# Optimization experiments

Measured on AMD Instinct MI355X. Metric: run time of the kernel, lower is better.

## Reference

```python
import jax, jax.numpy as jnp
import numpy as np

PATCH = 16

def setup_inputs() -> dict:
    key = jax.random.key(0)
    k1, k2, k3, k4, k5 = jax.random.split(key, 5)
    B, C, H, W = 128, 3, 224, 224
    N = (H // PATCH) * (W // PATCH)  # 196
    D = 768
    x = jax.random.normal(k1, (B, C, H, W), dtype=jnp.float32)
    ys = jax.random.randint(k2, (B, N), 0, H - PATCH + 1, dtype=jnp.int64)
    xs = jax.random.randint(k3, (B, N), 0, W - PATCH + 1, dtype=jnp.int64)
    W_proj = jax.random.normal(k4, (D, C * PATCH * PATCH), dtype=jnp.float32) * 0.02
    b_proj = jax.random.normal(k5, (D,), dtype=jnp.float32) * 0.02
    return {"x": x, "ys": ys, "xs": xs, "W_proj": W_proj, "b_proj": b_proj}

def reference(x, ys, xs, W_proj, b_proj):
    # x: [B, C, H, W]; ys, xs: [B, N] top-left patch coords
    B, C, H, W = x.shape
    N = ys.shape[1]
    P = PATCH
    # flattened within-patch offsets: d[p] = dy*W + dx, shape [P*P]
    dy = jnp.arange(P)[:, None]
    dx = jnp.arange(P)[None, :]
    d = (dy * W + dx).reshape(-1)  # [P*P]
    base = ys * W + xs                         # [B, N]
    indices = base[:, :, None] + d[None, None, :]  # [B, N, P*P]
    indices = indices.reshape(B, N * P * P)
    # gather over flattened spatial dims for every channel
    x_flat = x.reshape(B, C, H * W)
    patches = jnp.take_along_axis(
        x_flat, indices[:, None, :].astype(jnp.int32), axis=2
    )  # [B, C, N*P*P]
    patches = patches.reshape(B, C, N, P * P)
    patches = patches.transpose(0, 2, 1, 3).reshape(B, N, C * P * P)  # [B, N, C*P*P]
    patch_tokens = jnp.einsum('bnf,df->bnd', patches, W_proj) + b_proj  # [B, N, D]
    patch_positions = jnp.stack([ys, xs], axis=-1)  # [B, N, 2]
    return (patch_tokens, patch_positions)
```

## Files before the change

kernel.cpp:

```cpp
#include <hip/hip_runtime.h>
#include <hip/hip_bf16.h>

#define B_IMG   128
#define CH      3
#define HW      224
#define NPATCH  196
#define TOKENS  25088
#define PATCH   16
#define FDIM    768
#define DDIM    768
#define TOKELEMS ((size_t)TOKENS * FDIM)
#define OUT_TOKENS ((size_t)TOKENS * DDIM)

#define GATHER_BRICK_BLOCKS (37632 / 4)
#define W_BRICK_BLOCKS      (1152 / 4)

typedef short short8 __attribute__((ext_vector_type(8)));
typedef float f32x4  __attribute__((ext_vector_type(4)));

static __device__ __forceinline__ unsigned short f2bf(float v) {
  unsigned u = __float_as_uint(v);
  unsigned r = u + 0x7fffu + ((u >> 16) & 1u);
  return (unsigned short)(r >> 16);
}

__global__ __launch_bounds__(256) void prep_kernel(
    const float* __restrict__ x, const int* __restrict__ ys,
    const int* __restrict__ xs, const float* __restrict__ W,
    short* __restrict__ PF, short* __restrict__ WF,
    float* __restrict__ pos) {
  const int w  = threadIdx.x >> 6;
  const int l  = threadIdx.x & 63;
  const int lr = l & 15;
  const int lg = l >> 4;
  const int k8rem = lg & 3;

  if (blockIdx.x < GATHER_BRICK_BLOCKS) {
    const int brick  = blockIdx.x * 4 + w;
    const int tile16 = brick / 24;
    const int kt     = brick - tile16 * 24;
    const int tok    = tile16 * 16 + lr;
    const int b      = tok / NPATCH;
    const int y      = ys[tok];
    const int xc     = xs[tok];
    const int k8     = kt * 4 + k8rem;
    const int c      = k8 >> 5;
    const int rem    = k8 & 31;
    const int py     = rem >> 1;
    const int px0    = (rem & 1) * 8;
    const float* src = x + (size_t)(b * CH + c) * (HW * HW) +
                       (size_t)(y + py) * HW + xc + px0;
    float4 v0 = *(const float4*)src;
    float4 v1 = *(const float4*)(src + 4);
    short8 o;
    o[0] = (short)f2bf(v0.x); o[1] = (short)f2bf(v0.y);
    o[2] = (short)f2bf(v0.z); o[3] = (short)f2bf(v0.w);
    o[4] = (short)f2bf(v1.x); o[5] = (short)f2bf(v1.y);
    o[6] = (short)f2bf(v1.z); o[7] = (short)f2bf(v1.w);
    *(short8*)&PF[(size_t)brick * 512 + l * 8] = o;
    if (kt == 0 && lg == 0) {
      pos[(size_t)tok * 2]     = (float)y;
      pos[(size_t)tok * 2 + 1] = (float)xc;
    }
  } else {
    const int brick  = (blockIdx.x - GATHER_BRICK_BLOCKS) * 4 + w;
    const int tile16 = brick / 24;
    const int kt     = brick - tile16 * 24;
    const int n      = tile16 * 16 + lr;
    const int k8     = kt * 4 + k8rem;
    const float* src = W + (size_t)n * FDIM + k8 * 8;
    float4 v0 = *(const float4*)src;
    float4 v1 = *(const float4*)(src + 4);
    short8 o;
    o[0] = (short)f2bf(v0.x); o[1] = (short)f2bf(v0.y);
    o[2] = (short)f2bf(v0.z); o[3] = (short)f2bf(v0.w);
    o[4] = (short)f2bf(v1.x); o[5] = (short)f2bf(v1.y);
    o[6] = (short)f2bf(v1.z); o[7] = (short)f2bf(v1.w);
    *(short8*)&WF[(size_t)brick * 512 + l * 8] = o;
  }
}

__global__ __launch_bounds__(256) void gemm_kernel(
    const short* __restrict__ PF,
    const short* __restrict__ WF,
    const float* __restrict__ bias,
    float* __restrict__ C) {
  const int tid = threadIdx.x;
  const int w   = tid >> 6;
  const int l   = tid & 63;
  const int lr  = l & 15;
  const int lg  = l >> 4;

  const int id  = blockIdx.x;
  const int nid = (id & 7) * 147 + (id >> 3);
  const int job = nid * 4 + w;
  const int mt  = job / 12;
  const int nt  = job - mt * 12;
  const int m0  = mt * 64;
  const int n0  = nt * 64;

  const short* pA = PF + (size_t)(m0 >> 4) * 24 * 512 + l * 8;
  const short* pB = WF + (size_t)(n0 >> 4) * 24 * 512 + l * 8;

  float bs4[4];
#pragma unroll
  for (int ni = 0; ni < 4; ++ni) bs4[ni] = bias[n0 + ni * 16 + lr];
#pragma unroll
  for (int ni = 0; ni < 4; ++ni) asm volatile("" : "+v"(bs4[ni]));

  f32x4 acc[4][4];
  const f32x4 z = {0.f, 0.f, 0.f, 0.f};
#pragma unroll
  for (int mi = 0; mi < 4; ++mi)
#pragma unroll
    for (int ni = 0; ni < 4; ++ni) acc[mi][ni] = z;

  short8 A0[4], B0[4], A1[4], B1[4];

#define LOADSET(Af, Bf, KT)                                                  \
  do {                                                                       \
    const size_t ko_ = (size_t)(KT) * 512;                                   \
    _Pragma("unroll")                                                        \
    for (int i = 0; i < 4; ++i)                                              \
      Af[i] = *(const short8*)(pA + (size_t)i * 12288 + ko_);                \
    _Pragma("unroll")                                                        \
    for (int i = 0; i < 4; ++i)                                              \
      Bf[i] = *(const short8*)(pB + (size_t)i * 12288 + ko_);                \
  } while (0)

#define MFMASET(Af, Bf)                                                      \
  do {                                                                       \
    __builtin_amdgcn_s_setprio(1);                                           \
    _Pragma("unroll")                                                        \
    for (int mi = 0; mi < 4; ++mi)                                           \
      _Pragma("unroll")                                                      \
      for (int ni = 0; ni < 4; ++ni)                                         \
        acc[mi][ni] = __builtin_amdgcn_mfma_f32_16x16x32_bf16(               \
            Af[mi], Bf[ni], acc[mi][ni], 0, 0, 0);                           \
    __builtin_amdgcn_s_setprio(0);                                           \
  } while (0)

  LOADSET(A0, B0, 0);
#pragma unroll 1
  for (int s = 0; s < 24; s += 2) {
    LOADSET(A1, B1, s + 1);
    asm volatile("s_waitcnt vmcnt(8)" ::: "memory");
    MFMASET(A0, B0);
    const int k2 = (s + 2 < 24) ? s + 2 : 0;
    LOADSET(A0, B0, k2);
    asm volatile("s_waitcnt vmcnt(8)" ::: "memory");
    MFMASET(A1, B1);
  }

#pragma unroll
  for (int ni = 0; ni < 4; ++ni) {
    const int col = n0 + ni * 16 + lr;
#pragma unroll
    for (int mi = 0; mi < 4; ++mi) {
      const int row = m0 + mi * 16 + lg * 4;
      const f32x4 v = acc[mi][ni];
#pragma unroll
      for (int j = 0; j < 4; ++j)
        C[(size_t)(row + j) * DDIM + col] = v[j] + bs4[ni];
    }
  }
#undef LOADSET
#undef MFMASET
}

__global__ __launch_bounds__(256) void naive_kernel(
    const float* __restrict__ x, const int* __restrict__ ys,
    const int* __restrict__ xs, const float* __restrict__ W,
    const float* __restrict__ bias, float* __restrict__ out) {
  __shared__ float prow[FDIM];
  const int tok = blockIdx.x;
  const int t   = threadIdx.x;
  const int b   = tok / NPATCH;
  const int y   = ys[tok];
  const int xc  = xs[tok];
  for (int i = t; i < FDIM; i += 256) {
    int c = i >> 8, rem = i & 255, py = rem >> 4, px = rem & 15;
    prow[i] = x[((size_t)(b * CH + c) * HW + y + py) * HW + xc + px];
  }
  __syncthreads();
  for (int dd = 0; dd < 3; ++dd) {
    const int d = t + dd * 256;
    float s = bias[d];
    const float4* wr = (const float4*)&W[(size_t)d * FDIM];
    const float4* pr = (const float4*)prow;
    for (int f4 = 0; f4 < FDIM / 4; ++f4) {
      float4 wv = wr[f4];
      float4 pv = pr[f4];
      s += wv.x * pv.x + wv.y * pv.y + wv.z * pv.z + wv.w * pv.w;
    }
    out[(size_t)tok * DDIM + d] = s;
  }
  if (t == 0) {
    float* pos = out + OUT_TOKENS;
    pos[(size_t)tok * 2]     = (float)y;
    pos[(size_t)tok * 2 + 1] = (float)xc;
  }
}

extern "C" void kernel_launch(void* const* d_in, const int* in_sizes, int n_in,
                              void* d_out, int out_size, void* d_ws, size_t ws_size,
                              hipStream_t stream) {
  const float* x    = (const float*)d_in[0];
  const int*   ys   = (const int*)d_in[1];
  const int*   xs   = (const int*)d_in[2];
  const float* W    = (const float*)d_in[3];
  const float* bias = (const float*)d_in[4];
  float* out = (float*)d_out;
  float* pos = out + OUT_TOKENS;

  const size_t w_bytes = (size_t)DDIM * FDIM * 2;
  const size_t p_bytes = TOKELEMS * 2;
  if (ws_size >= w_bytes + p_bytes) {
    short* WF = (short*)d_ws;
    short* PF = (short*)d_ws + (size_t)DDIM * FDIM;
    prep_kernel<<<GATHER_BRICK_BLOCKS + W_BRICK_BLOCKS, 256, 0, stream>>>(
        x, ys, xs, W, PF, WF, pos);
    gemm_kernel<<<1176, 256, 0, stream>>>(PF, WF, bias, out);
  } else {
    naive_kernel<<<TOKENS, 256, 0, stream>>>(x, ys, xs, W, bias, out);
  }
}
```

Baseline: 75.66 us.

## Share A tiles across waves via LDS triple buffer, enlarge block tile to 128x256

The GEMM moves from independent 64x64 per-wave tiles loaded straight from global memory to a 128x256 block tile. The A operand is staged through a three-slot LDS buffer with direct global-to-LDS loads and shared by all four waves, while each wave keeps its own B fragments in registers. The grid halves and the XCD-aware block mapping is adjusted to the new count. This cuts redundant global/L2 traffic for A, at the cost of more accumulator registers (32 f32x4), per-step barriers, and lower occupancy.

```diff
diff --git a/kernel.cpp b/kernel.cpp
--- a/kernel.cpp
+++ b/kernel.cpp
@@ -22,6 +22,13 @@
   unsigned u = __float_as_uint(v);
   unsigned r = u + 0x7fffu + ((u >> 16) & 1u);
   return (unsigned short)(r >> 16);
+}
+
+static __device__ __forceinline__ void gload16(const short* g, short* l) {
+  __builtin_amdgcn_global_load_lds(
+      (const __attribute__((address_space(1))) void*)g,
+      (__attribute__((address_space(3))) void*)l,
+      16, 0, 0);
 }
 
 __global__ __launch_bounds__(256) void prep_kernel(
@@ -85,22 +92,26 @@
     const short* __restrict__ WF,
     const float* __restrict__ bias,
     float* __restrict__ C) {
+  __shared__ short Ab[3][8 * 512];
+
   const int tid = threadIdx.x;
   const int w   = tid >> 6;
   const int l   = tid & 63;
   const int lr  = l & 15;
   const int lg  = l >> 4;
 
-  const int id  = blockIdx.x;
-  const int nid = (id & 7) * 147 + (id >> 3);
-  const int job = nid * 4 + w;
-  const int mt  = job / 12;
-  const int nt  = job - mt * 12;
-  const int m0  = mt * 64;
-  const int n0  = nt * 64;
-
-  const short* pA = PF + (size_t)(m0 >> 4) * 24 * 512 + l * 8;
+  const int id   = blockIdx.x;
+  const int xcd  = id & 7;
+  const int chnk = id >> 3;
+  const int nid  = (xcd < 4 ? xcd * 74 : 296 + (xcd - 4) * 73) + chnk;
+  const int mtB  = nid / 3;
+  const int ntg  = nid - mtB * 3;
+  const int m0   = mtB * 128;
+  const int n0   = ntg * 256 + w * 64;
+
   const short* pB = WF + (size_t)(n0 >> 4) * 24 * 512 + l * 8;
+  const short* pAs = PF + (size_t)(mtB * 8 + w * 2) * 24 * 512 + l * 8;
+  const int ldst = (w * 2) * 512;
 
   float bs4[4];
 #pragma unroll
@@ -108,55 +119,92 @@
 #pragma unroll
   for (int ni = 0; ni < 4; ++ni) asm volatile("" : "+v"(bs4[ni]));
 
-  f32x4 acc[4][4];
+  f32x4 acc[8][4];
   const f32x4 z = {0.f, 0.f, 0.f, 0.f};
 #pragma unroll
-  for (int mi = 0; mi < 4; ++mi)
+  for (int mi = 0; mi < 8; ++mi)
 #pragma unroll
     for (int ni = 0; ni < 4; ++ni) acc[mi][ni] = z;
 
-  short8 A0[4], B0[4], A1[4], B1[4];
-
-#define LOADSET(Af, Bf, KT)                                                  \
-  do {                                                                       \
-    const size_t ko_ = (size_t)(KT) * 512;                                   \
-    _Pragma("unroll")                                                        \
-    for (int i = 0; i < 4; ++i)                                              \
-      Af[i] = *(const short8*)(pA + (size_t)i * 12288 + ko_);                \
-    _Pragma("unroll")                                                        \
-    for (int i = 0; i < 4; ++i)                                              \
-      Bf[i] = *(const short8*)(pB + (size_t)i * 12288 + ko_);                \
+  short8 B0[4], B1[4];
+
+#define LOADB(BR, KT)                                                      \
+  do {                                                                     \
+    _Pragma("unroll")                                                      \
+    for (int i = 0; i < 4; ++i)                                            \
+      BR[i] = *(const short8*)(pB + (size_t)i * 12288 + (size_t)(KT) * 512);\
   } while (0)
 
-#define MFMASET(Af, Bf)                                                      \
-  do {                                                                       \
-    __builtin_amdgcn_s_setprio(1);                                           \
-    _Pragma("unroll")                                                        \
-    for (int mi = 0; mi < 4; ++mi)                                           \
-      _Pragma("unroll")                                                      \
-      for (int ni = 0; ni < 4; ++ni)                                         \
-        acc[mi][ni] = __builtin_amdgcn_mfma_f32_16x16x32_bf16(               \
-            Af[mi], Bf[ni], acc[mi][ni], 0, 0, 0);                           \
-    __builtin_amdgcn_s_setprio(0);                                           \
+#define STAGEA(SLOT, KT)                                                   \
+  do {                                                                     \
+    gload16(pAs + (size_t)(KT) * 512, &Ab[(SLOT)][ldst]);                  \
+    gload16(pAs + 12288 + (size_t)(KT) * 512, &Ab[(SLOT)][ldst + 512]);    \
   } while (0)
 
-  LOADSET(A0, B0, 0);
+#define GSTEP(BUF, STG, BR, KT2, DOSTG, DOB, VMN)                          \
+  do {                                                                     \
+    short8 a_[4];                                                          \
+    _Pragma("unroll")                                                      \
+    for (int i = 0; i < 4; ++i)                                            \
+      a_[i] = *(const short8*)&Ab[(BUF)][i * 512 + l * 8];                 \
+    if (DOSTG) STAGEA(STG, KT2);                                           \
+    asm volatile("s_waitcnt vmcnt(" #VMN ")" ::: "memory");                \
+    __builtin_amdgcn_sched_barrier(0);                                     \
+    __builtin_amdgcn_s_setprio(1);                                         \
+    _Pragma("unroll")                                                      \
+    for (int mi = 0; mi < 4; ++mi)                                         \
+      _Pragma("unroll")                                                    \
+      for (int ni = 0; ni < 4; ++ni)                                       \
+        acc[mi][ni] = __builtin_amdgcn_mfma_f32_16x16x32_bf16(             \
+            a_[mi], BR[ni], acc[mi][ni], 0, 0, 0);                         \
+    __builtin_amdgcn_s_setprio(0);                                         \
+    short8 a2_[4];                                                         \
+    _Pragma("unroll")                                                      \
+    for (int i = 0; i < 4; ++i)                                            \
+      a2_[i] = *(const short8*)&Ab[(BUF)][(4 + i) * 512 + l * 8];          \
+    __builtin_amdgcn_s_setprio(1);                                         \
+    _Pragma("unroll")                                                      \
+    for (int mi = 0; mi < 4; ++mi)                                         \
+      _Pragma("unroll")                                                    \
+      for (int ni = 0; ni < 4; ++ni)                                       \
+        acc[4 + mi][ni] = __builtin_amdgcn_mfma_f32_16x16x32_bf16(         \
+            a2_[mi], BR[ni], acc[4 + mi][ni], 0, 0, 0);                    \
+    __builtin_amdgcn_s_setprio(0);                                         \
+    if (DOB) LOADB(BR, KT2);                                               \
+    __builtin_amdgcn_sched_barrier(0);                                     \
+    __builtin_amdgcn_s_barrier();                                          \
+  } while (0)
+
+  STAGEA(0, 0);
+  LOADB(B0, 0);
+  STAGEA(1, 1);
+  LOADB(B1, 1);
+  asm volatile("s_waitcnt vmcnt(10)" ::: "memory");
+  __builtin_amdgcn_sched_barrier(0);
+  __builtin_amdgcn_s_barrier();
+
 #pragma unroll 1
-  for (int s = 0; s < 24; s += 2) {
-    LOADSET(A1, B1, s + 1);
-    asm volatile("s_waitcnt vmcnt(8)" ::: "memory");
-    MFMASET(A0, B0);
-    const int k2 = (s + 2 < 24) ? s + 2 : 0;
-    LOADSET(A0, B0, k2);
-    asm volatile("s_waitcnt vmcnt(8)" ::: "memory");
-    MFMASET(A1, B1);
-  }
+  for (int p = 0; p < 3; ++p) {
+    const int s0 = p * 6;
+    GSTEP(0, 2, B0, s0 + 2, 1, 1, 6);
+    GSTEP(1, 0, B1, s0 + 3, 1, 1, 6);
+    GSTEP(2, 1, B0, s0 + 4, 1, 1, 6);
+    GSTEP(0, 2, B1, s0 + 5, 1, 1, 6);
+    GSTEP(1, 0, B0, s0 + 6, 1, 1, 6);
+    GSTEP(2, 1, B1, s0 + 7, 1, 1, 6);
+  }
+  GSTEP(0, 2, B0, 20, 1, 1, 6);
+  GSTEP(1, 0, B1, 21, 1, 1, 6);
+  GSTEP(2, 1, B0, 22, 1, 1, 6);
+  GSTEP(0, 2, B1, 23, 1, 1, 6);
+  GSTEP(1, 0, B0, 24, 0, 0, 4);
+  GSTEP(2, 1, B1, 25, 0, 0, 0);
 
 #pragma unroll
   for (int ni = 0; ni < 4; ++ni) {
     const int col = n0 + ni * 16 + lr;
 #pragma unroll
-    for (int mi = 0; mi < 4; ++mi) {
+    for (int mi = 0; mi < 8; ++mi) {
       const int row = m0 + mi * 16 + lg * 4;
       const f32x4 v = acc[mi][ni];
 #pragma unroll
@@ -164,8 +212,9 @@
         C[(size_t)(row + j) * DDIM + col] = v[j] + bs4[ni];
     }
   }
-#undef LOADSET
-#undef MFMASET
+#undef LOADB
+#undef STAGEA
+#undef GSTEP
 }
 
 __global__ __launch_bounds__(256) void naive_kernel(
@@ -220,7 +269,7 @@
     short* PF = (short*)d_ws + (size_t)DDIM * FDIM;
     prep_kernel<<<GATHER_BRICK_BLOCKS + W_BRICK_BLOCKS, 256, 0, stream>>>(
         x, ys, xs, W, PF, WF, pos);
-    gemm_kernel<<<1176, 256, 0, stream>>>(PF, WF, bias, out);
+    gemm_kernel<<<588, 256, 0, stream>>>(PF, WF, bias, out);
   } else {
     naive_kernel<<<TOKENS, 256, 0, stream>>>(x, ys, xs, W, bias, out);
   }
```

New measurement: 75.96 us. No clear change (+0.4%).
